# Performance work log

Measured on AMD Instinct MI355X. Metric: run time of the kernel, lower is better.

Reference implementation:

```python
import jax, jax.numpy as jnp
import numpy as np

TAU = 1.0
SCALE = 0.5
LN_EPS = 1e-5
NORM_EPS = 1e-12


def setup_inputs() -> dict:
    key = jax.random.key(0)
    k1, = jax.random.split(key, 1)
    N, D = 16384, 128
    x = jax.random.normal(k1, (N, D), dtype=jnp.float32)
    gamma = jnp.ones((D,), dtype=jnp.float32)
    beta = jnp.zeros((D,), dtype=jnp.float32)
    return {"x": x, "gamma": gamma, "beta": beta}


def reference(x, gamma, beta):
    # 'cn' branch: row-normalize, full pairwise cosine sim, row softmax, aggregate
    norm = jnp.sqrt(jnp.sum(x * x, axis=1, keepdims=True))
    norm_x = x / jnp.maximum(norm, NORM_EPS)          # [N, D]
    sim = jax.nn.softmax(norm_x @ norm_x.T / TAU, axis=1)  # [N, N]
    x_neg = sim @ x                                    # [N, D]
    y = (1.0 + SCALE) * x - SCALE * x_neg
    # LayerNorm over the hidden dim
    mu = jnp.mean(y, axis=-1, keepdims=True)
    var = jnp.mean((y - mu) ** 2, axis=-1, keepdims=True)
    return (y - mu) * jax.lax.rsqrt(var + LN_EPS) * gamma + beta
```

## Files before the change

### kernel.cpp

```cpp
#include <hip/hip_runtime.h>
#include <stdint.h>

#define NN 16384
#define DD 128
#define KT 64
#define QB 128
#define KSTR 144
#define VSTR 72
#define KBYTES 9216
#define VBYTES 9216

typedef float f32x16 __attribute__((ext_vector_type(16)));
typedef int i32x8 __attribute__((ext_vector_type(8)));

using gv = __attribute__((address_space(1))) const void;
using lv = __attribute__((address_space(3))) void;

__device__ __forceinline__ i32x8 mk8(uint4 a, uint4 b) {
  i32x8 r;
  r[0] = a.x; r[1] = a.y; r[2] = a.z; r[3] = a.w;
  r[4] = b.x; r[5] = b.y; r[6] = b.z; r[7] = b.w;
  return r;
}

#define MFMA64(A, B, C) \
  __builtin_amdgcn_mfma_scale_f32_32x32x64_f8f6f4((A), (B), (C), 0, 0, 0, 0x7F7F7F7F, 0, 0x7F7F7F7F)

__global__ void k_norm(const float* __restrict__ x, uint8_t* __restrict__ nx) {
  const int wave = threadIdx.x >> 6, lane = threadIdx.x & 63;
  const int row = blockIdx.x * 4 + wave;
  const float2 v = *reinterpret_cast<const float2*>(x + (size_t)row * DD + 2 * lane);
  float ss = v.x * v.x + v.y * v.y;
#pragma unroll
  for (int m = 1; m < 64; m <<= 1) ss += __shfl_xor(ss, m);
  const float rn = 1.2011224087f / fmaxf(sqrtf(ss), 1e-12f);
  const int w = __builtin_amdgcn_cvt_pk_fp8_f32(v.x * rn, v.y * rn, 0, false);
  *reinterpret_cast<uint16_t*>(nx + (size_t)row * DD + 2 * lane) = (uint16_t)w;
}

__global__ void k_transpose(const float* __restrict__ x, uint8_t* __restrict__ xT) {
  __shared__ uint16_t tile[64 * 66];
  const int n0 = blockIdx.x * 64;
  const int t = threadIdx.x;
#pragma unroll
  for (int e = 0; e < 16; ++e) {
    const int idx = e * 256 + t;
    const int r = idx >> 6, c2 = idx & 63;
    const float2 v = *reinterpret_cast<const float2*>(x + (size_t)(n0 + r) * DD + 2 * c2);
    const int w = __builtin_amdgcn_cvt_pk_fp8_f32(v.x, v.y, 0, false);
    tile[r * 66 + c2] = (uint16_t)w;
  }
  __syncthreads();
  const uint8_t* t8 = reinterpret_cast<const uint8_t*>(tile);
#pragma unroll
  for (int e = 0; e < 8; ++e) {
    const int idx = e * 256 + t;
    const int d = idx >> 4, n4 = (idx & 15) << 2;
    uint32_t w = (uint32_t)t8[(n4 + 0) * 132 + d];
    w |= (uint32_t)t8[(n4 + 1) * 132 + d] << 8;
    w |= (uint32_t)t8[(n4 + 2) * 132 + d] << 16;
    w |= (uint32_t)t8[(n4 + 3) * 132 + d] << 24;
    *reinterpret_cast<uint32_t*>(xT + (size_t)d * NN + n0 + n4) = w;
  }
}

template <int NSPLIT>
__global__ __launch_bounds__(256, 4) void k_attn(
    const uint8_t* __restrict__ nx, const uint8_t* __restrict__ xT,
    float* __restrict__ Op, float* __restrict__ Lp) {
  __shared__ alignas(16) uint8_t Kb[2][KBYTES];
  __shared__ alignas(16) uint8_t Vb[2][VBYTES];

  const int tid = threadIdx.x;
  const int wave = tid >> 6;
  const int lane = tid & 63;
  const int rl = lane & 31;
  const int hi = lane >> 5;

  const int id = blockIdx.x;
  constexpr int gs = 8 / NSPLIT;
  const int split = (id & 7) / gs;
  const int qblock = (id >> 3) * gs + (id & (gs - 1));

  constexpr int nt = 256 / NSPLIT;
  const int t0s = split * nt;
  const int qw = qblock * QB + wave * 32;

  const int sw = wave >> 1;
  const int j0 = (wave & 1) * 5;
  const int cnt = (wave & 1) ? 4 : 5;
  uint32_t soff[5];
#pragma unroll
  for (int i = 0; i < 5; ++i) {
    const int j = j0 + i;
    const int t16 = j * 64 + lane;
    if (sw == 0) {
      soff[i] = (uint32_t)((t16 / 9) * DD + (t16 % 9) * 16);
    } else {
      const int d = (2 * t16) / 9;
      const int c0 = t16 * 16 - d * VSTR;
      soff[i] = (uint32_t)(d * NN + c0 + (c0 >= 64 ? (NN - VSTR) : 0));
    }
  }

  auto stage = [&](int tt, int buf) {
    const int k0 = tt * KT;
    const uint8_t* basep = (sw == 0) ? (nx + (size_t)k0 * DD) : (xT + k0);
    uint8_t* ldsb = (sw == 0) ? &Kb[buf][0] : &Vb[buf][0];
#pragma unroll
    for (int i = 0; i < 5; ++i)
      if (i < cnt)
        __builtin_amdgcn_global_load_lds((gv*)(basep + soff[i]),
            (lv*)(ldsb + (j0 + i) * 1024), 16, 0, 0);
  };

  const uint8_t* qrow = nx + (size_t)(qw + rl) * DD + 32 * hi;
  i32x8 q8[2];
#pragma unroll
  for (int c = 0; c < 2; ++c)
    q8[c] = mk8(*reinterpret_cast<const uint4*>(qrow + c * 64),
                *reinterpret_cast<const uint4*>(qrow + c * 64 + 16));

  f32x16 o[4];
#pragma unroll
  for (int dt = 0; dt < 4; ++dt)
#pragma unroll
    for (int r = 0; r < 16; ++r) o[dt][r] = 0.f;
  float lsum = 0.f;

  stage(t0s, 0);

  for (int t = 0; t < nt; ++t) {
    const int buf = t & 1;
    __builtin_amdgcn_sched_barrier(0);
    asm volatile("s_waitcnt vmcnt(0)" ::: "memory");
    __builtin_amdgcn_sched_barrier(0);
    __builtin_amdgcn_s_barrier();
    __builtin_amdgcn_sched_barrier(0);
    if (t + 1 < nt) stage(t0s + t + 1, buf ^ 1);

    const uint8_t* kb = &Kb[buf][0];
    const uint8_t* vb = &Vb[buf][0];

    uint32_t W0[4], W1[4];
#pragma unroll
    for (int kt = 0; kt < 2; ++kt) {
      const uint8_t* kbb = kb + kt * 32 * KSTR + rl * KSTR + 32 * hi;
      const i32x8 ka0 = mk8(*reinterpret_cast<const uint4*>(kbb),
                            *reinterpret_cast<const uint4*>(kbb + 16));
      const i32x8 ka1 = mk8(*reinterpret_cast<const uint4*>(kbb + 64),
                            *reinterpret_cast<const uint4*>(kbb + 80));
      f32x16 s = {};
      s = MFMA64(ka0, q8[0], s);
      s = MFMA64(ka1, q8[1], s);
      float e[16];
#pragma unroll
      for (int r = 0; r < 16; ++r) {
        float p;
        asm("v_exp_f32 %0, %1" : "=v"(p) : "v"(s[r]));
        e[r] = p;
        lsum += p;
      }
      uint32_t* W = kt ? W1 : W0;
#pragma unroll
      for (int g = 0; g < 4; ++g) {
        uint32_t w = (uint32_t)__builtin_amdgcn_cvt_pk_fp8_f32(e[4 * g + 0], e[4 * g + 1], 0, false);
        w = (uint32_t)__builtin_amdgcn_cvt_pk_fp8_f32(e[4 * g + 2], e[4 * g + 3], (int)w, true);
        W[g] = w;
      }
    }
#pragma unroll
    for (int g = 0; g < 4; ++g)
      asm("v_permlane32_swap_b32 %0, %1" : "+v"(W0[g]), "+v"(W1[g]));
    i32x8 pa;
    pa[0] = (int)W0[0]; pa[1] = (int)W1[0]; pa[2] = (int)W0[1]; pa[3] = (int)W1[1];
    pa[4] = (int)W0[2]; pa[5] = (int)W1[2]; pa[6] = (int)W0[3]; pa[7] = (int)W1[3];

#pragma unroll
    for (int dt = 0; dt < 4; ++dt) {
      const uint8_t* vp = vb + (dt * 32 + rl) * VSTR + 32 * hi;
      const i32x8 vf = mk8(*reinterpret_cast<const uint4*>(vp),
                           *reinterpret_cast<const uint4*>(vp + 16));
      o[dt] = MFMA64(pa, vf, o[dt]);
    }
  }

  const float lt = lsum + __shfl_xor(lsum, 32);
  if (hi == 0) Lp[(size_t)split * NN + qw + rl] = lt;

  float* Ob = Op + (size_t)split * NN * DD;
#pragma unroll
  for (int dt = 0; dt < 4; ++dt)
#pragma unroll
    for (int r = 0; r < 16; ++r) {
      const int q = (r & 3) + 8 * (r >> 2) + 4 * hi;
      Ob[(size_t)(qw + q) * DD + dt * 32 + rl] = o[dt][r];
    }
}

__global__ void k_final(const float* __restrict__ x, const float* __restrict__ gamma,
                        const float* __restrict__ beta, const float* __restrict__ Op,
                        const float* __restrict__ Lp, float* __restrict__ out, int nsplit) {
  const int wave = threadIdx.x >> 6, lane = threadIdx.x & 63;
  const int row = blockIdx.x * 4 + wave;
  float o0 = 0.f, o1 = 0.f, lt = 0.f;
  for (int s = 0; s < nsplit; ++s) {
    const float2 v = *reinterpret_cast<const float2*>(
        Op + (size_t)s * NN * DD + (size_t)row * DD + 2 * lane);
    o0 += v.x;
    o1 += v.y;
    lt += Lp[(size_t)s * NN + row];
  }
  const float inv = 1.0f / lt;
  const float2 xv = *reinterpret_cast<const float2*>(x + (size_t)row * DD + 2 * lane);
  float y0 = 1.5f * xv.x - 0.5f * o0 * inv;
  float y1 = 1.5f * xv.y - 0.5f * o1 * inv;
  float sum = y0 + y1;
#pragma unroll
  for (int m = 1; m < 64; m <<= 1) sum += __shfl_xor(sum, m);
  const float mu = sum * (1.0f / 128.0f);
  const float d0 = y0 - mu, d1 = y1 - mu;
  float vs = d0 * d0 + d1 * d1;
#pragma unroll
  for (int m = 1; m < 64; m <<= 1) vs += __shfl_xor(vs, m);
  const float rs = rsqrtf(vs * (1.0f / 128.0f) + 1e-5f);
  const float2 g = *reinterpret_cast<const float2*>(gamma + 2 * lane);
  const float2 b = *reinterpret_cast<const float2*>(beta + 2 * lane);
  float2 ov;
  ov.x = d0 * rs * g.x + b.x;
  ov.y = d1 * rs * g.y + b.y;
  *reinterpret_cast<float2*>(out + (size_t)row * DD + 2 * lane) = ov;
}

extern "C" void kernel_launch(void* const* d_in, const int* in_sizes, int n_in,
                              void* d_out, int out_size, void* d_ws, size_t ws_size,
                              hipStream_t stream) {
  const float* x = (const float*)d_in[0];
  const float* gamma = (const float*)d_in[1];
  const float* beta = (const float*)d_in[2];
  float* out = (float*)d_out;
  char* ws = (char*)d_ws;

  uint8_t* nx = (uint8_t*)ws;
  uint8_t* xT = (uint8_t*)(ws + (size_t)NN * DD);
  const size_t base = (size_t)2 * NN * DD;
  const size_t per = (size_t)NN * DD * 4 + (size_t)NN * 4;

  int nsplit = 2;
  if (ws_size >= base + 8 * per) nsplit = 8;
  else if (ws_size >= base + 4 * per) nsplit = 4;

  float* Op = (float*)(ws + base);
  float* Lp = (float*)(ws + base + (size_t)nsplit * NN * DD * 4);

  k_norm<<<NN / 4, 256, 0, stream>>>(x, nx);
  k_transpose<<<NN / 64, 256, 0, stream>>>(x, xT);
  if (nsplit == 8)
    k_attn<8><<<dim3(128 * 8), 256, 0, stream>>>(nx, xT, Op, Lp);
  else if (nsplit == 4)
    k_attn<4><<<dim3(128 * 4), 256, 0, stream>>>(nx, xT, Op, Lp);
  else
    k_attn<2><<<dim3(128 * 2), 256, 0, stream>>>(nx, xT, Op, Lp);
  k_final<<<NN / 4, 256, 0, stream>>>(x, gamma, beta, Op, Lp, out, nsplit);
}
```

Before: 165.6 us.

## Load K/V tiles directly from global into registers, dropping LDS staging

Removes the double-buffered LDS staging of K and V tiles, along with its async global-to-LDS copies and per-iteration barrier and waitcnt. Each wave now reads its MFMA operand fragments straight from global memory, relying on L2/L1 caching because all four waves share the same K/V tiles. Launch bounds drop from 4 to 3 blocks per SM to allow more registers. The trade-off is redundant global traffic across waves, strided V reads, and no explicit prefetch overlap.

```diff
diff --git a/kernel.cpp b/kernel.cpp
--- a/kernel.cpp
+++ b/kernel.cpp
@@ -5,16 +5,9 @@
 #define DD 128
 #define KT 64
 #define QB 128
-#define KSTR 144
-#define VSTR 72
-#define KBYTES 9216
-#define VBYTES 9216
 
 typedef float f32x16 __attribute__((ext_vector_type(16)));
 typedef int i32x8 __attribute__((ext_vector_type(8)));
-
-using gv = __attribute__((address_space(1))) const void;
-using lv = __attribute__((address_space(3))) void;
 
 __device__ __forceinline__ i32x8 mk8(uint4 a, uint4 b) {
   i32x8 r;
@@ -65,12 +58,9 @@
 }
 
 template <int NSPLIT>
-__global__ __launch_bounds__(256, 4) void k_attn(
+__global__ __launch_bounds__(256, 3) void k_attn(
     const uint8_t* __restrict__ nx, const uint8_t* __restrict__ xT,
     float* __restrict__ Op, float* __restrict__ Lp) {
-  __shared__ alignas(16) uint8_t Kb[2][KBYTES];
-  __shared__ alignas(16) uint8_t Vb[2][VBYTES];
-
   const int tid = threadIdx.x;
   const int wave = tid >> 6;
   const int lane = tid & 63;
@@ -86,34 +76,6 @@
   const int t0s = split * nt;
   const int qw = qblock * QB + wave * 32;
 
-  const int sw = wave >> 1;
-  const int j0 = (wave & 1) * 5;
-  const int cnt = (wave & 1) ? 4 : 5;
-  uint32_t soff[5];
-#pragma unroll
-  for (int i = 0; i < 5; ++i) {
-    const int j = j0 + i;
-    const int t16 = j * 64 + lane;
-    if (sw == 0) {
-      soff[i] = (uint32_t)((t16 / 9) * DD + (t16 % 9) * 16);
-    } else {
-      const int d = (2 * t16) / 9;
-      const int c0 = t16 * 16 - d * VSTR;
-      soff[i] = (uint32_t)(d * NN + c0 + (c0 >= 64 ? (NN - VSTR) : 0));
-    }
-  }
-
-  auto stage = [&](int tt, int buf) {
-    const int k0 = tt * KT;
-    const uint8_t* basep = (sw == 0) ? (nx + (size_t)k0 * DD) : (xT + k0);
-    uint8_t* ldsb = (sw == 0) ? &Kb[buf][0] : &Vb[buf][0];
-#pragma unroll
-    for (int i = 0; i < 5; ++i)
-      if (i < cnt)
-        __builtin_amdgcn_global_load_lds((gv*)(basep + soff[i]),
-            (lv*)(ldsb + (j0 + i) * 1024), 16, 0, 0);
-  };
-
   const uint8_t* qrow = nx + (size_t)(qw + rl) * DD + 32 * hi;
   i32x8 q8[2];
 #pragma unroll
@@ -128,28 +90,40 @@
     for (int r = 0; r < 16; ++r) o[dt][r] = 0.f;
   float lsum = 0.f;
 
-  stage(t0s, 0);
+  const uint8_t* kbase = nx + (size_t)rl * DD + 32 * hi;
+  const uint8_t* vbase = xT + 32 * hi;
 
   for (int t = 0; t < nt; ++t) {
-    const int buf = t & 1;
-    __builtin_amdgcn_sched_barrier(0);
-    asm volatile("s_waitcnt vmcnt(0)" ::: "memory");
-    __builtin_amdgcn_sched_barrier(0);
-    __builtin_amdgcn_s_barrier();
-    __builtin_amdgcn_sched_barrier(0);
-    if (t + 1 < nt) stage(t0s + t + 1, buf ^ 1);
-
-    const uint8_t* kb = &Kb[buf][0];
-    const uint8_t* vb = &Vb[buf][0];
+    const int k0 = (t0s + t) * KT;
+
+    const uint8_t* kp0 = kbase + (size_t)k0 * DD;
+    const uint8_t* kp1 = kp0 + 32 * DD;
+    const uint4 k0a = *reinterpret_cast<const uint4*>(kp0);
+    const uint4 k0b = *reinterpret_cast<const uint4*>(kp0 + 16);
+    const uint4 k0c = *reinterpret_cast<const uint4*>(kp0 + 64);
+    const uint4 k0d = *reinterpret_cast<const uint4*>(kp0 + 80);
+    const uint4 k1a = *reinterpret_cast<const uint4*>(kp1);
+    const uint4 k1b = *reinterpret_cast<const uint4*>(kp1 + 16);
+    const uint4 k1c = *reinterpret_cast<const uint4*>(kp1 + 64);
+    const uint4 k1d = *reinterpret_cast<const uint4*>(kp1 + 80);
+    const uint8_t* vp0 = vbase + (size_t)(0 * 32 + rl) * NN + k0;
+    const uint8_t* vp1 = vbase + (size_t)(1 * 32 + rl) * NN + k0;
+    const uint8_t* vp2 = vbase + (size_t)(2 * 32 + rl) * NN + k0;
+    const uint8_t* vp3 = vbase + (size_t)(3 * 32 + rl) * NN + k0;
+    const uint4 v0a = *reinterpret_cast<const uint4*>(vp0);
+    const uint4 v0b = *reinterpret_cast<const uint4*>(vp0 + 16);
+    const uint4 v1a = *reinterpret_cast<const uint4*>(vp1);
+    const uint4 v1b = *reinterpret_cast<const uint4*>(vp1 + 16);
+    const uint4 v2a = *reinterpret_cast<const uint4*>(vp2);
+    const uint4 v2b = *reinterpret_cast<const uint4*>(vp2 + 16);
+    const uint4 v3a = *reinterpret_cast<const uint4*>(vp3);
+    const uint4 v3b = *reinterpret_cast<const uint4*>(vp3 + 16);
 
     uint32_t W0[4], W1[4];
 #pragma unroll
     for (int kt = 0; kt < 2; ++kt) {
-      const uint8_t* kbb = kb + kt * 32 * KSTR + rl * KSTR + 32 * hi;
-      const i32x8 ka0 = mk8(*reinterpret_cast<const uint4*>(kbb),
-                            *reinterpret_cast<const uint4*>(kbb + 16));
-      const i32x8 ka1 = mk8(*reinterpret_cast<const uint4*>(kbb + 64),
-                            *reinterpret_cast<const uint4*>(kbb + 80));
+      const i32x8 ka0 = kt ? mk8(k1a, k1b) : mk8(k0a, k0b);
+      const i32x8 ka1 = kt ? mk8(k1c, k1d) : mk8(k0c, k0d);
       f32x16 s = {};
       s = MFMA64(ka0, q8[0], s);
       s = MFMA64(ka1, q8[1], s);
@@ -176,13 +150,10 @@
     pa[0] = (int)W0[0]; pa[1] = (int)W1[0]; pa[2] = (int)W0[1]; pa[3] = (int)W1[1];
     pa[4] = (int)W0[2]; pa[5] = (int)W1[2]; pa[6] = (int)W0[3]; pa[7] = (int)W1[3];
 
-#pragma unroll
-    for (int dt = 0; dt < 4; ++dt) {
-      const uint8_t* vp = vb + (dt * 32 + rl) * VSTR + 32 * hi;
-      const i32x8 vf = mk8(*reinterpret_cast<const uint4*>(vp),
-                           *reinterpret_cast<const uint4*>(vp + 16));
-      o[dt] = MFMA64(pa, vf, o[dt]);
-    }
+    o[0] = MFMA64(pa, mk8(v0a, v0b), o[0]);
+    o[1] = MFMA64(pa, mk8(v1a, v1b), o[1]);
+    o[2] = MFMA64(pa, mk8(v2a, v2b), o[2]);
+    o[3] = MFMA64(pa, mk8(v3a, v3b), o[3]);
   }
 
   const float lt = lsum + __shfl_xor(lsum, 32);
```

New measurement: 289.1 us. 74.6% more time.

## Stage 128-key phases per barrier with staggered start and interleaved QK/PV

Applied to the files above, without the earlier changes.

The attention loop now stages 128 keys per iteration instead of 64, into a unified LDS buffer (two K tiles, two V tiles, each wave loading one tile). This halves the number of barrier/waitcnt synchronizations and lets QK MFMAs for two sub-tiles issue before the exp/pack and PV work. Blocks also start at a staggered phase offset to spread L2/HBM access across key ranges. The max split count drops from 8 to 4 and launch bounds go to 2 blocks/CU, trading occupancy and parallelism for more work per sync, with LDS use doubling to about 72KB per block.

```diff
diff --git a/kernel.cpp b/kernel.cpp
--- a/kernel.cpp
+++ b/kernel.cpp
@@ -3,12 +3,10 @@
 
 #define NN 16384
 #define DD 128
-#define KT 64
 #define QB 128
 #define KSTR 144
 #define VSTR 72
-#define KBYTES 9216
-#define VBYTES 9216
+#define TBYTES 9216
 
 typedef float f32x16 __attribute__((ext_vector_type(16)));
 typedef int i32x8 __attribute__((ext_vector_type(8)));
@@ -25,6 +23,7 @@
 
 #define MFMA64(A, B, C) \
   __builtin_amdgcn_mfma_scale_f32_32x32x64_f8f6f4((A), (B), (C), 0, 0, 0, 0x7F7F7F7F, 0, 0x7F7F7F7F)
+#define LD16(p) (*reinterpret_cast<const uint4*>(p))
 
 __global__ void k_norm(const float* __restrict__ x, uint8_t* __restrict__ nx) {
   const int wave = threadIdx.x >> 6, lane = threadIdx.x & 63;
@@ -64,12 +63,59 @@
   }
 }
 
+#define QKT(kb_, s0_, s1_)                                                \
+  {                                                                       \
+    const uint8_t* kbb_ = (kb_) + rl * KSTR + 32 * hi;                    \
+    i32x8 a_;                                                             \
+    a_ = mk8(LD16(kbb_), LD16(kbb_ + 16));                                \
+    s0_ = MFMA64(a_, q80, s0_);                                           \
+    a_ = mk8(LD16(kbb_ + 64), LD16(kbb_ + 80));                           \
+    s0_ = MFMA64(a_, q81, s0_);                                           \
+    const uint8_t* kb1_ = kbb_ + 32 * KSTR;                               \
+    a_ = mk8(LD16(kb1_), LD16(kb1_ + 16));                                \
+    s1_ = MFMA64(a_, q80, s1_);                                           \
+    a_ = mk8(LD16(kb1_ + 64), LD16(kb1_ + 80));                           \
+    s1_ = MFMA64(a_, q81, s1_);                                           \
+  }
+
+#define SMPACK(sv_, W_)                                                   \
+  {                                                                       \
+    _Pragma("unroll") for (int g = 0; g < 4; ++g) {                       \
+      float e0_, e1_, e2_, e3_;                                           \
+      asm("v_exp_f32 %0, %1" : "=v"(e0_) : "v"(sv_[4 * g + 0]));          \
+      asm("v_exp_f32 %0, %1" : "=v"(e1_) : "v"(sv_[4 * g + 1]));          \
+      asm("v_exp_f32 %0, %1" : "=v"(e2_) : "v"(sv_[4 * g + 2]));          \
+      asm("v_exp_f32 %0, %1" : "=v"(e3_) : "v"(sv_[4 * g + 3]));          \
+      lsum += (e0_ + e1_) + (e2_ + e3_);                                  \
+      uint32_t w_ = (uint32_t)__builtin_amdgcn_cvt_pk_fp8_f32(e0_, e1_, 0, false); \
+      w_ = (uint32_t)__builtin_amdgcn_cvt_pk_fp8_f32(e2_, e3_, (int)w_, true);     \
+      W_[g] = w_;                                                         \
+    }                                                                     \
+  }
+
+#define MKPA(pa_, W0_, W1_)                                               \
+  _Pragma("unroll") for (int g = 0; g < 4; ++g)                           \
+      asm("v_permlane32_swap_b32 %0, %1" : "+v"(W0_[g]), "+v"(W1_[g]));   \
+  i32x8 pa_;                                                              \
+  pa_[0] = (int)W0_[0]; pa_[1] = (int)W1_[0];                             \
+  pa_[2] = (int)W0_[1]; pa_[3] = (int)W1_[1];                             \
+  pa_[4] = (int)W0_[2]; pa_[5] = (int)W1_[2];                             \
+  pa_[6] = (int)W0_[3]; pa_[7] = (int)W1_[3];
+
+#define PVT(vb_, pa_)                                                     \
+  {                                                                       \
+    const uint8_t* vp_ = (vb_) + rl * VSTR + 32 * hi;                     \
+    o[0] = MFMA64(pa_, mk8(LD16(vp_), LD16(vp_ + 16)), o[0]);             \
+    o[1] = MFMA64(pa_, mk8(LD16(vp_ + 32 * VSTR), LD16(vp_ + 32 * VSTR + 16)), o[1]); \
+    o[2] = MFMA64(pa_, mk8(LD16(vp_ + 64 * VSTR), LD16(vp_ + 64 * VSTR + 16)), o[2]); \
+    o[3] = MFMA64(pa_, mk8(LD16(vp_ + 96 * VSTR), LD16(vp_ + 96 * VSTR + 16)), o[3]); \
+  }
+
 template <int NSPLIT>
-__global__ __launch_bounds__(256, 4) void k_attn(
+__global__ __launch_bounds__(256, 2) void k_attn(
     const uint8_t* __restrict__ nx, const uint8_t* __restrict__ xT,
     float* __restrict__ Op, float* __restrict__ Lp) {
-  __shared__ alignas(16) uint8_t Kb[2][KBYTES];
-  __shared__ alignas(16) uint8_t Vb[2][VBYTES];
+  __shared__ alignas(16) uint8_t LDSU[2][4][TBYTES];
 
   const int tid = threadIdx.x;
   const int wave = tid >> 6;
@@ -81,20 +127,17 @@
   constexpr int gs = 8 / NSPLIT;
   const int split = (id & 7) / gs;
   const int qblock = (id >> 3) * gs + (id & (gs - 1));
-
-  constexpr int nt = 256 / NSPLIT;
-  const int t0s = split * nt;
+  constexpr int nph = 128 / NSPLIT;
+  const int r0s = split * (NN / NSPLIT);
+  const int pst = ((id >> 3) + ((id >> 8) << 4)) & (nph - 1);
   const int qw = qblock * QB + wave * 32;
 
-  const int sw = wave >> 1;
-  const int j0 = (wave & 1) * 5;
-  const int cnt = (wave & 1) ? 4 : 5;
-  uint32_t soff[5];
-#pragma unroll
-  for (int i = 0; i < 5; ++i) {
-    const int j = j0 + i;
-    const int t16 = j * 64 + lane;
-    if (sw == 0) {
+  const bool isK = wave < 2;
+  uint32_t soff[9];
+#pragma unroll
+  for (int i = 0; i < 9; ++i) {
+    const int t16 = i * 64 + lane;
+    if (isK) {
       soff[i] = (uint32_t)((t16 / 9) * DD + (t16 % 9) * 16);
     } else {
       const int d = (2 * t16) / 9;
@@ -102,24 +145,21 @@
       soff[i] = (uint32_t)(d * NN + c0 + (c0 >= 64 ? (NN - VSTR) : 0));
     }
   }
-
-  auto stage = [&](int tt, int buf) {
-    const int k0 = tt * KT;
-    const uint8_t* basep = (sw == 0) ? (nx + (size_t)k0 * DD) : (xT + k0);
-    uint8_t* ldsb = (sw == 0) ? &Kb[buf][0] : &Vb[buf][0];
-#pragma unroll
-    for (int i = 0; i < 5; ++i)
-      if (i < cnt)
-        __builtin_amdgcn_global_load_lds((gv*)(basep + soff[i]),
-            (lv*)(ldsb + (j0 + i) * 1024), 16, 0, 0);
+  const int woff = (wave & 1) * 64;
+
+  auto stage = [&](int phm, int buf) {
+    const size_t r0 = (size_t)r0s + (size_t)phm * 128 + woff;
+    const uint8_t* basep = isK ? (nx + r0 * DD) : (xT + r0);
+    uint8_t* ldsb = &LDSU[buf][wave][0];
+#pragma unroll
+    for (int i = 0; i < 9; ++i)
+      __builtin_amdgcn_global_load_lds((gv*)(basep + soff[i]),
+          (lv*)(ldsb + i * 1024), 16, 0, 0);
   };
 
   const uint8_t* qrow = nx + (size_t)(qw + rl) * DD + 32 * hi;
-  i32x8 q8[2];
-#pragma unroll
-  for (int c = 0; c < 2; ++c)
-    q8[c] = mk8(*reinterpret_cast<const uint4*>(qrow + c * 64),
-                *reinterpret_cast<const uint4*>(qrow + c * 64 + 16));
+  const i32x8 q80 = mk8(LD16(qrow), LD16(qrow + 16));
+  const i32x8 q81 = mk8(LD16(qrow + 64), LD16(qrow + 80));
 
   f32x16 o[4];
 #pragma unroll
@@ -128,61 +168,41 @@
     for (int r = 0; r < 16; ++r) o[dt][r] = 0.f;
   float lsum = 0.f;
 
-  stage(t0s, 0);
-
-  for (int t = 0; t < nt; ++t) {
-    const int buf = t & 1;
+  stage(pst, 0);
+
+  for (int pp = 0; pp < nph; ++pp) {
+    const int buf = pp & 1;
+    int pc = pp + pst;
+    if (pc >= nph) pc -= nph;
+
     __builtin_amdgcn_sched_barrier(0);
     asm volatile("s_waitcnt vmcnt(0)" ::: "memory");
     __builtin_amdgcn_sched_barrier(0);
     __builtin_amdgcn_s_barrier();
     __builtin_amdgcn_sched_barrier(0);
-    if (t + 1 < nt) stage(t0s + t + 1, buf ^ 1);
-
-    const uint8_t* kb = &Kb[buf][0];
-    const uint8_t* vb = &Vb[buf][0];
-
-    uint32_t W0[4], W1[4];
-#pragma unroll
-    for (int kt = 0; kt < 2; ++kt) {
-      const uint8_t* kbb = kb + kt * 32 * KSTR + rl * KSTR + 32 * hi;
-      const i32x8 ka0 = mk8(*reinterpret_cast<const uint4*>(kbb),
-                            *reinterpret_cast<const uint4*>(kbb + 16));
-      const i32x8 ka1 = mk8(*reinterpret_cast<const uint4*>(kbb + 64),
-                            *reinterpret_cast<const uint4*>(kbb + 80));
-      f32x16 s = {};
-      s = MFMA64(ka0, q8[0], s);
-      s = MFMA64(ka1, q8[1], s);
-      float e[16];
-#pragma unroll
-      for (int r = 0; r < 16; ++r) {
-        float p;
-        asm("v_exp_f32 %0, %1" : "=v"(p) : "v"(s[r]));
-        e[r] = p;
-        lsum += p;
-      }
-      uint32_t* W = kt ? W1 : W0;
-#pragma unroll
-      for (int g = 0; g < 4; ++g) {
-        uint32_t w = (uint32_t)__builtin_amdgcn_cvt_pk_fp8_f32(e[4 * g + 0], e[4 * g + 1], 0, false);
-        w = (uint32_t)__builtin_amdgcn_cvt_pk_fp8_f32(e[4 * g + 2], e[4 * g + 3], (int)w, true);
-        W[g] = w;
-      }
+    if (pp + 1 < nph) {
+      int pn = pc + 1;
+      if (pn >= nph) pn -= nph;
+      stage(pn, buf ^ 1);
     }
-#pragma unroll
-    for (int g = 0; g < 4; ++g)
-      asm("v_permlane32_swap_b32 %0, %1" : "+v"(W0[g]), "+v"(W1[g]));
-    i32x8 pa;
-    pa[0] = (int)W0[0]; pa[1] = (int)W1[0]; pa[2] = (int)W0[1]; pa[3] = (int)W1[1];
-    pa[4] = (int)W0[2]; pa[5] = (int)W1[2]; pa[6] = (int)W0[3]; pa[7] = (int)W1[3];
-
-#pragma unroll
-    for (int dt = 0; dt < 4; ++dt) {
-      const uint8_t* vp = vb + (dt * 32 + rl) * VSTR + 32 * hi;
-      const i32x8 vf = mk8(*reinterpret_cast<const uint4*>(vp),
-                           *reinterpret_cast<const uint4*>(vp + 16));
-      o[dt] = MFMA64(pa, vf, o[dt]);
-    }
+
+    const uint8_t* kA = &LDSU[buf][0][0];
+    const uint8_t* kB = &LDSU[buf][1][0];
+    const uint8_t* vA = &LDSU[buf][2][0];
+    const uint8_t* vB = &LDSU[buf][3][0];
+
+    f32x16 sA0 = {}, sA1 = {}, sB0 = {}, sB1 = {};
+    QKT(kA, sA0, sA1);
+    QKT(kB, sB0, sB1);
+    uint32_t WA0[4], WA1[4], WB0[4], WB1[4];
+    SMPACK(sA0, WA0);
+    SMPACK(sA1, WA1);
+    MKPA(paA, WA0, WA1);
+    PVT(vA, paA);
+    SMPACK(sB0, WB0);
+    SMPACK(sB1, WB1);
+    MKPA(paB, WB0, WB1);
+    PVT(vB, paB);
   }
 
   const float lt = lsum + __shfl_xor(lsum, 32);
@@ -247,17 +267,14 @@
   const size_t per = (size_t)NN * DD * 4 + (size_t)NN * 4;
 
   int nsplit = 2;
-  if (ws_size >= base + 8 * per) nsplit = 8;
-  else if (ws_size >= base + 4 * per) nsplit = 4;
+  if (ws_size >= base + 4 * per) nsplit = 4;
 
   float* Op = (float*)(ws + base);
   float* Lp = (float*)(ws + base + (size_t)nsplit * NN * DD * 4);
 
   k_norm<<<NN / 4, 256, 0, stream>>>(x, nx);
   k_transpose<<<NN / 64, 256, 0, stream>>>(x, xT);
-  if (nsplit == 8)
-    k_attn<8><<<dim3(128 * 8), 256, 0, stream>>>(nx, xT, Op, Lp);
-  else if (nsplit == 4)
+  if (nsplit == 4)
     k_attn<4><<<dim3(128 * 4), 256, 0, stream>>>(nx, xT, Op, Lp);
   else
     k_attn<2><<<dim3(128 * 2), 256, 0, stream>>>(nx, xT, Op, Lp);
```

Result: faster. 157.7 us (-4.8%).
